# Kernel optimization log

Hardware: AMD Instinct MI355X
Metric: run time of the kernel (lower is better)

The kernel has to match this reference:

```python
import jax, jax.numpy as jnp
import numpy as np

D = 128
N = 100000
E = 500000
DIM_OUT = 2


def setup_inputs() -> dict:
    key = jax.random.key(0)
    ks = jax.random.split(key, 12)
    s = lambda d: 1.0 / np.sqrt(d)
    return {
        "x": jax.random.normal(ks[0], (N, D), jnp.float32),
        "edge_attr": jax.random.normal(ks[1], (E, D), jnp.float32),
        # node head MLP: D -> D -> DIM_OUT
        "W1": jax.random.uniform(ks[2], (D, D), jnp.float32, -s(D), s(D)),
        "b1": jnp.zeros((D,), jnp.float32),
        "W2": jax.random.uniform(ks[3], (D, DIM_OUT), jnp.float32, -s(D), s(D)),
        "b2": jnp.zeros((DIM_OUT,), jnp.float32),
        # edge aux head MLP: 3D -> 3D -> 1
        "V1": jax.random.uniform(ks[4], (3 * D, 3 * D), jnp.float32, -s(3 * D), s(3 * D)),
        "bv1": jnp.zeros((3 * D,), jnp.float32),
        "V2": jax.random.uniform(ks[5], (3 * D, 1), jnp.float32, -s(3 * D), s(3 * D)),
        "bv2": jnp.zeros((1,), jnp.float32),
        "edge_combine_weight": jnp.asarray(0.5, jnp.float32),
        "edge_index": jax.random.randint(ks[6], (2, E), 0, N, jnp.int64),
        "y": jax.random.randint(ks[7], (N,), 0, 2, jnp.int64),
        "batch_size": 50000,
    }


def reference(x, edge_attr, W1, b1, W2, b2, V1, bv1, V2, bv2,
              edge_combine_weight, edge_index, y, batch_size):
    # node classification head: 2-layer MLP
    node_logits = jax.nn.relu(x @ W1 + b1) @ W2 + b2  # [N, 2]

    src, dst = edge_index[0], edge_index[1]
    # gather src/dst node embeddings, concat edge attrs -> [E, 3D]
    edge_input = jnp.concatenate([x[src], x[dst], edge_attr], axis=-1)
    edge_scores = (jax.nn.relu(edge_input @ V1 + bv1) @ V2 + bv2)[:, 0]  # [E]
    edge_sig = jax.nn.sigmoid(edge_scores)

    # scatter-max into node slots; empty slots -> 0 (torch_scatter semantics)
    signal = jax.ops.segment_max(edge_sig, src, num_segments=N)
    signal = jnp.where(jnp.isfinite(signal), signal, 0.0)

    node_logits = node_logits.at[:, 1].add(edge_combine_weight * signal)

    pred = node_logits[:batch_size]
    label = y[:batch_size]
    return pred, label
```

## Files before the change

kernel.cpp:

```cpp
#include <hip/hip_runtime.h>
#include <hip/hip_bf16.h>

typedef __bf16 bf16;
typedef bf16 bf16x8 __attribute__((ext_vector_type(8)));
typedef float f32x4 __attribute__((ext_vector_type(4)));

#define D 128

__global__ void prep_kernel(const float* __restrict__ V1, const float* __restrict__ W1,
                            bf16* __restrict__ V1t, bf16* __restrict__ W1t) {
  int i = blockIdx.x * 256 + threadIdx.x;
  if (i < 384 * 384) { int k = i / 384, n = i % 384; V1t[n * 384 + k] = (bf16)V1[i]; }
  if (i < 128 * 128) { int k = i >> 7, n = i & 127;  W1t[n * 128 + k] = (bf16)W1[i]; }
}

__global__ void compact_kernel(const int* __restrict__ ei, int E, int bs,
                               int* __restrict__ count, int* __restrict__ list) {
  int e = blockIdx.x * 256 + threadIdx.x;
  if (e < E && ei[e] < bs) {
    int p = atomicAdd(count, 1);
    list[p] = e;
  }
}

__global__ __launch_bounds__(256, 2) void node_kernel(
    const float* __restrict__ x, const bf16* __restrict__ W1t,
    const float* __restrict__ b1, const float* __restrict__ W2,
    const float* __restrict__ b2, float* __restrict__ logits, int bs)
{
  __shared__ bf16 sA[64][136];
  __shared__ float sOut0[64], sOut1[64];

  int tid = threadIdx.x;
  if (tid < 64) { sOut0[tid] = 0.f; sOut1[tid] = 0.f; }

  {
    int g = tid >> 5, fl = tid & 31;
#pragma unroll
    for (int i = 0; i < 8; ++i) {
      int row = i * 8 + g;
      const float4* base = (const float4*)(x + (size_t)(blockIdx.x * 64 + row) * D);
      float4 v = base[fl];
      union { bf16 h[4]; uint2 u; } cv;
      cv.h[0] = (bf16)v.x; cv.h[1] = (bf16)v.y; cv.h[2] = (bf16)v.z; cv.h[3] = (bf16)v.w;
      *(uint2*)&sA[row][fl * 4] = cv.u;
    }
  }
  __syncthreads();

  int wave = tid >> 6, lane = tid & 63;
  int l15 = lane & 15, quad = lane >> 4;

  f32x4 acc[2][4];
#pragma unroll
  for (int ct = 0; ct < 2; ++ct)
#pragma unroll
    for (int rt = 0; rt < 4; ++rt)
      acc[ct][rt] = (f32x4){0.f, 0.f, 0.f, 0.f};

  for (int kc = 0; kc < 4; ++kc) {
    int k = kc * 32 + quad * 8;
    bf16x8 a[4], b[2];
#pragma unroll
    for (int rt = 0; rt < 4; ++rt)
      a[rt] = *(const bf16x8*)&sA[rt * 16 + l15][k];
#pragma unroll
    for (int ct = 0; ct < 2; ++ct)
      b[ct] = *(const bf16x8*)&W1t[(size_t)(wave * 32 + ct * 16 + l15) * 128 + k];
#pragma unroll
    for (int ct = 0; ct < 2; ++ct)
#pragma unroll
      for (int rt = 0; rt < 4; ++rt)
        acc[ct][rt] = __builtin_amdgcn_mfma_f32_16x16x32_bf16(a[rt], b[ct], acc[ct][rt], 0, 0, 0);
  }

  float bc[2], w0[2], w1[2];
#pragma unroll
  for (int ct = 0; ct < 2; ++ct) {
    int n = wave * 32 + ct * 16 + l15;
    bc[ct] = b1[n]; w0[ct] = W2[n * 2]; w1[ct] = W2[n * 2 + 1];
  }
#pragma unroll
  for (int rt = 0; rt < 4; ++rt) {
#pragma unroll
    for (int reg = 0; reg < 4; ++reg) {
      float p0 = 0.f, p1 = 0.f;
#pragma unroll
      for (int ct = 0; ct < 2; ++ct) {
        float h = fmaxf(acc[ct][rt][reg] + bc[ct], 0.f);
        p0 += h * w0[ct]; p1 += h * w1[ct];
      }
      p0 += __shfl_xor(p0, 1, 16); p0 += __shfl_xor(p0, 2, 16);
      p0 += __shfl_xor(p0, 4, 16); p0 += __shfl_xor(p0, 8, 16);
      p1 += __shfl_xor(p1, 1, 16); p1 += __shfl_xor(p1, 2, 16);
      p1 += __shfl_xor(p1, 4, 16); p1 += __shfl_xor(p1, 8, 16);
      if (l15 == 0) {
        int row = rt * 16 + quad * 4 + reg;
        atomicAdd(&sOut0[row], p0);
        atomicAdd(&sOut1[row], p1);
      }
    }
  }
  __syncthreads();
  if (tid < 64) {
    int node = blockIdx.x * 64 + tid;
    if (node < bs) {
      logits[2 * node]     = sOut0[tid] + b2[0];
      logits[2 * node + 1] = sOut1[tid] + b2[1];
    }
  }
}

__global__ __launch_bounds__(256, 2) void edge_kernel(
    const float* __restrict__ x, const float* __restrict__ ea,
    const bf16* __restrict__ V1t, const float* __restrict__ bv1,
    const float* __restrict__ V2, const float* __restrict__ bv2,
    const int* __restrict__ ei, const int* __restrict__ count,
    const int* __restrict__ list, float* __restrict__ signal,
    int E, int bs)
{
  __shared__ bf16 sA[64][392];
  __shared__ float sScore[64];
  __shared__ int sSrc[64], sDst[64], sE[64];

  int nvalid = *count - (int)(blockIdx.x * 64);
  if (nvalid <= 0) return;
  if (nvalid > 64) nvalid = 64;

  int tid = threadIdx.x;
  if (tid < 64) {
    int e = 0;
    if (tid < nvalid) e = list[blockIdx.x * 64 + tid];
    sE[tid] = e;
    sSrc[tid] = ei[e];
    sDst[tid] = ei[E + e];
    sScore[tid] = 0.f;
  }
  __syncthreads();

  {
    int g = tid >> 5, fl = tid & 31;
#pragma unroll
    for (int i = 0; i < 24; ++i) {
      int t = i * 8 + g;
      int row = t & 63, seg = t >> 6;
      const float* base;
      if (seg == 0)      base = x  + (size_t)sSrc[row] * D;
      else if (seg == 1) base = x  + (size_t)sDst[row] * D;
      else               base = ea + (size_t)sE[row]   * D;
      float4 v = ((const float4*)base)[fl];
      union { bf16 h[4]; uint2 u; } cv;
      cv.h[0] = (bf16)v.x; cv.h[1] = (bf16)v.y; cv.h[2] = (bf16)v.z; cv.h[3] = (bf16)v.w;
      *(uint2*)&sA[row][seg * 128 + fl * 4] = cv.u;
    }
  }
  __syncthreads();

  int wave = tid >> 6, lane = tid & 63;
  int l15 = lane & 15, quad = lane >> 4;

  f32x4 acc[6][4];
#pragma unroll
  for (int ct = 0; ct < 6; ++ct)
#pragma unroll
    for (int rt = 0; rt < 4; ++rt)
      acc[ct][rt] = (f32x4){0.f, 0.f, 0.f, 0.f};

  const bf16* Bbase = V1t + (size_t)(wave * 96 + l15) * 384 + quad * 8;

  for (int kc = 0; kc < 12; ++kc) {
    int k = kc * 32 + quad * 8;
    bf16x8 a[4], b[6];
#pragma unroll
    for (int rt = 0; rt < 4; ++rt)
      a[rt] = *(const bf16x8*)&sA[rt * 16 + l15][k];
#pragma unroll
    for (int ct = 0; ct < 6; ++ct)
      b[ct] = *(const bf16x8*)(Bbase + (size_t)ct * 16 * 384 + kc * 32);
#pragma unroll
    for (int ct = 0; ct < 6; ++ct)
#pragma unroll
      for (int rt = 0; rt < 4; ++rt)
        acc[ct][rt] = __builtin_amdgcn_mfma_f32_16x16x32_bf16(a[rt], b[ct], acc[ct][rt], 0, 0, 0);
  }

  float bvc[6], v2c[6];
#pragma unroll
  for (int ct = 0; ct < 6; ++ct) {
    int n = wave * 96 + ct * 16 + l15;
    bvc[ct] = bv1[n]; v2c[ct] = V2[n];
  }
#pragma unroll
  for (int rt = 0; rt < 4; ++rt) {
#pragma unroll
    for (int reg = 0; reg < 4; ++reg) {
      float p = 0.f;
#pragma unroll
      for (int ct = 0; ct < 6; ++ct)
        p += fmaxf(acc[ct][rt][reg] + bvc[ct], 0.f) * v2c[ct];
      p += __shfl_xor(p, 1, 16);
      p += __shfl_xor(p, 2, 16);
      p += __shfl_xor(p, 4, 16);
      p += __shfl_xor(p, 8, 16);
      if (l15 == 0)
        atomicAdd(&sScore[rt * 16 + quad * 4 + reg], p);
    }
  }
  __syncthreads();
  if (tid < nvalid) {
    float sc = sScore[tid] + bv2[0];
    float sig = 1.f / (1.f + __expf(-sc));
    atomicMax((int*)&signal[sSrc[tid]], __float_as_int(sig));
  }
}

__global__ void combine_kernel(const float* __restrict__ logits, const float* __restrict__ signal,
                               const int* __restrict__ y, const float* __restrict__ ecw,
                               float* __restrict__ out, int bs) {
  int i = blockIdx.x * 256 + threadIdx.x;
  if (i < bs) {
    out[2 * i]     = logits[2 * i];
    out[2 * i + 1] = logits[2 * i + 1] + ecw[0] * signal[i];
    out[2 * bs + i] = (float)y[i];
  }
}

extern "C" void kernel_launch(void* const* d_in, const int* in_sizes, int n_in,
                              void* d_out, int out_size, void* d_ws, size_t ws_size,
                              hipStream_t stream) {
  const float* x   = (const float*)d_in[0];
  const float* ea  = (const float*)d_in[1];
  const float* W1  = (const float*)d_in[2];
  const float* b1  = (const float*)d_in[3];
  const float* W2  = (const float*)d_in[4];
  const float* b2  = (const float*)d_in[5];
  const float* V1  = (const float*)d_in[6];
  const float* bv1 = (const float*)d_in[7];
  const float* V2  = (const float*)d_in[8];
  const float* bv2 = (const float*)d_in[9];
  const float* ecw = (const float*)d_in[10];
  const int*   ei  = (const int*)d_in[11];
  const int*   y   = (const int*)d_in[12];

  int E  = in_sizes[1] / D;
  int bs = out_size / 3;

  char* ws = (char*)d_ws;
  size_t off = 0;
  bf16* V1t = (bf16*)(ws + off); off += (size_t)384 * 384 * 2;
  bf16* W1t = (bf16*)(ws + off); off += (size_t)128 * 128 * 2;
  float* signal = (float*)(ws + off); off += (size_t)bs * 4;
  float* logits = (float*)(ws + off); off += (size_t)bs * 8;
  int* count = (int*)(ws + off); off += 16;
  int* list  = (int*)(ws + off); off += (size_t)E * 4;

  hipMemsetAsync(signal, 0, (size_t)bs * 4, stream);
  hipMemsetAsync(count, 0, 4, stream);

  prep_kernel<<<(384 * 384 + 255) / 256, 256, 0, stream>>>(V1, W1, V1t, W1t);
  compact_kernel<<<(E + 255) / 256, 256, 0, stream>>>(ei, E, bs, count, list);
  node_kernel<<<(bs + 63) / 64, 256, 0, stream>>>(x, W1t, b1, W2, b2, logits, bs);
  edge_kernel<<<(E + 63) / 64, 256, 0, stream>>>(x, ea, V1t, bv1, V2, bv2,
                                                 ei, count, list, signal, E, bs);
  combine_kernel<<<(bs + 255) / 256, 256, 0, stream>>>(logits, signal, y, ecw,
                                                       (float*)d_out, bs);
}
```

Before: 682.7 us.

## Fuse setup kernels and make edge kernel persistent with prefetched gathers

Merges weight prep, edge compaction, node MLP and signal zeroing into one block-partitioned setup kernel, so the node MLP transposes W1 into shared memory itself. The edge kernel becomes a persistent grid of fixed size that loops over edge tiles, double-buffering gathered indices and prefetching the next tile's edge attributes and indices while computing the current one. It also software-pipelines the V1 B-operand loads across the k loop. This targets launch overhead and exposed gather latency, at the cost of more register pressure and a fixed grid size that may underfill or overfill the GPU.

Result: slower. 697.6 us (+2.2%).

```diff
diff --git a/kernel.cpp b/kernel.cpp
--- a/kernel.cpp
+++ b/kernel.cpp
@@ -6,108 +6,119 @@
 typedef float f32x4 __attribute__((ext_vector_type(4)));
 
 #define D 128
-
-__global__ void prep_kernel(const float* __restrict__ V1, const float* __restrict__ W1,
-                            bf16* __restrict__ V1t, bf16* __restrict__ W1t) {
-  int i = blockIdx.x * 256 + threadIdx.x;
-  if (i < 384 * 384) { int k = i / 384, n = i % 384; V1t[n * 384 + k] = (bf16)V1[i]; }
-  if (i < 128 * 128) { int k = i >> 7, n = i & 127;  W1t[n * 128 + k] = (bf16)W1[i]; }
-}
-
-__global__ void compact_kernel(const int* __restrict__ ei, int E, int bs,
-                               int* __restrict__ count, int* __restrict__ list) {
-  int e = blockIdx.x * 256 + threadIdx.x;
-  if (e < E && ei[e] < bs) {
-    int p = atomicAdd(count, 1);
-    list[p] = e;
-  }
-}
-
-__global__ __launch_bounds__(256, 2) void node_kernel(
-    const float* __restrict__ x, const bf16* __restrict__ W1t,
+#define EGRID 512
+
+__global__ __launch_bounds__(256) void setup_kernel(
+    const float* __restrict__ x, const float* __restrict__ W1,
     const float* __restrict__ b1, const float* __restrict__ W2,
-    const float* __restrict__ b2, float* __restrict__ logits, int bs)
+    const float* __restrict__ b2, const float* __restrict__ V1,
+    const int* __restrict__ ei, int E, int bs,
+    bf16* __restrict__ V1t, int* __restrict__ count, int* __restrict__ list,
+    float* __restrict__ signal, float* __restrict__ logits,
+    int NN, int NT, int NC)
 {
-  __shared__ bf16 sA[64][136];
-  __shared__ float sOut0[64], sOut1[64];
-
-  int tid = threadIdx.x;
-  if (tid < 64) { sOut0[tid] = 0.f; sOut1[tid] = 0.f; }
-
-  {
-    int g = tid >> 5, fl = tid & 31;
-#pragma unroll
-    for (int i = 0; i < 8; ++i) {
-      int row = i * 8 + g;
-      const float4* base = (const float4*)(x + (size_t)(blockIdx.x * 64 + row) * D);
-      float4 v = base[fl];
-      union { bf16 h[4]; uint2 u; } cv;
-      cv.h[0] = (bf16)v.x; cv.h[1] = (bf16)v.y; cv.h[2] = (bf16)v.z; cv.h[3] = (bf16)v.w;
-      *(uint2*)&sA[row][fl * 4] = cv.u;
-    }
-  }
-  __syncthreads();
-
-  int wave = tid >> 6, lane = tid & 63;
-  int l15 = lane & 15, quad = lane >> 4;
-
-  f32x4 acc[2][4];
-#pragma unroll
-  for (int ct = 0; ct < 2; ++ct)
-#pragma unroll
-    for (int rt = 0; rt < 4; ++rt)
-      acc[ct][rt] = (f32x4){0.f, 0.f, 0.f, 0.f};
-
-  for (int kc = 0; kc < 4; ++kc) {
-    int k = kc * 32 + quad * 8;
-    bf16x8 a[4], b[2];
-#pragma unroll
-    for (int rt = 0; rt < 4; ++rt)
-      a[rt] = *(const bf16x8*)&sA[rt * 16 + l15][k];
+  __shared__ struct { bf16 A[64][136]; bf16 W[128][136]; float o0[64]; float o1[64]; } sm;
+  int bid = blockIdx.x, tid = threadIdx.x;
+
+  if (bid < NN) {
+#pragma unroll
+    for (int p = 0; p < 4; ++p) {
+      int tile = tid + p * 256;
+      int tk = tile >> 5, tn = tile & 31;
+      float4 r0 = *(const float4*)&W1[(4 * tk + 0) * D + 4 * tn];
+      float4 r1 = *(const float4*)&W1[(4 * tk + 1) * D + 4 * tn];
+      float4 r2 = *(const float4*)&W1[(4 * tk + 2) * D + 4 * tn];
+      float4 r3 = *(const float4*)&W1[(4 * tk + 3) * D + 4 * tn];
+      const float* q0 = (const float*)&r0; const float* q1 = (const float*)&r1;
+      const float* q2 = (const float*)&r2; const float* q3 = (const float*)&r3;
+#pragma unroll
+      for (int j = 0; j < 4; ++j) {
+        union { bf16 h[4]; ushort4 u; } cv;
+        cv.h[0] = (bf16)q0[j]; cv.h[1] = (bf16)q1[j];
+        cv.h[2] = (bf16)q2[j]; cv.h[3] = (bf16)q3[j];
+        *(ushort4*)&sm.W[4 * tn + j][4 * tk] = cv.u;
+      }
+    }
+    {
+      int g = tid >> 5, fl = tid & 31;
+#pragma unroll
+      for (int i = 0; i < 8; ++i) {
+        int row = i * 8 + g;
+        const float4* base = (const float4*)(x + (size_t)(bid * 64 + row) * D);
+        float4 v = base[fl];
+        union { bf16 h[4]; uint2 u; } cv;
+        cv.h[0] = (bf16)v.x; cv.h[1] = (bf16)v.y; cv.h[2] = (bf16)v.z; cv.h[3] = (bf16)v.w;
+        *(uint2*)&sm.A[row][fl * 4] = cv.u;
+      }
+    }
+    if (tid < 64) { sm.o0[tid] = 0.f; sm.o1[tid] = 0.f; }
+    __syncthreads();
+
+    int wave = tid >> 6, lane = tid & 63;
+    int l15 = lane & 15, quad = lane >> 4;
+    f32x4 acc[2][4];
 #pragma unroll
     for (int ct = 0; ct < 2; ++ct)
-      b[ct] = *(const bf16x8*)&W1t[(size_t)(wave * 32 + ct * 16 + l15) * 128 + k];
-#pragma unroll
-    for (int ct = 0; ct < 2; ++ct)
-#pragma unroll
-      for (int rt = 0; rt < 4; ++rt)
-        acc[ct][rt] = __builtin_amdgcn_mfma_f32_16x16x32_bf16(a[rt], b[ct], acc[ct][rt], 0, 0, 0);
-  }
-
-  float bc[2], w0[2], w1[2];
-#pragma unroll
-  for (int ct = 0; ct < 2; ++ct) {
-    int n = wave * 32 + ct * 16 + l15;
-    bc[ct] = b1[n]; w0[ct] = W2[n * 2]; w1[ct] = W2[n * 2 + 1];
-  }
-#pragma unroll
-  for (int rt = 0; rt < 4; ++rt) {
-#pragma unroll
-    for (int reg = 0; reg < 4; ++reg) {
-      float p0 = 0.f, p1 = 0.f;
-#pragma unroll
-      for (int ct = 0; ct < 2; ++ct) {
-        float h = fmaxf(acc[ct][rt][reg] + bc[ct], 0.f);
-        p0 += h * w0[ct]; p1 += h * w1[ct];
-      }
-      p0 += __shfl_xor(p0, 1, 16); p0 += __shfl_xor(p0, 2, 16);
-      p0 += __shfl_xor(p0, 4, 16); p0 += __shfl_xor(p0, 8, 16);
-      p1 += __shfl_xor(p1, 1, 16); p1 += __shfl_xor(p1, 2, 16);
-      p1 += __shfl_xor(p1, 4, 16); p1 += __shfl_xor(p1, 8, 16);
-      if (l15 == 0) {
-        int row = rt * 16 + quad * 4 + reg;
-        atomicAdd(&sOut0[row], p0);
-        atomicAdd(&sOut1[row], p1);
-      }
-    }
-  }
-  __syncthreads();
-  if (tid < 64) {
-    int node = blockIdx.x * 64 + tid;
-    if (node < bs) {
-      logits[2 * node]     = sOut0[tid] + b2[0];
-      logits[2 * node + 1] = sOut1[tid] + b2[1];
-    }
+#pragma unroll
+      for (int rt = 0; rt < 4; ++rt) acc[ct][rt] = (f32x4){0.f, 0.f, 0.f, 0.f};
+    for (int kc = 0; kc < 4; ++kc) {
+      int k = kc * 32 + quad * 8;
+      bf16x8 a[4], b[2];
+#pragma unroll
+      for (int rt = 0; rt < 4; ++rt) a[rt] = *(const bf16x8*)&sm.A[rt * 16 + l15][k];
+#pragma unroll
+      for (int ct = 0; ct < 2; ++ct) b[ct] = *(const bf16x8*)&sm.W[wave * 32 + ct * 16 + l15][k];
+#pragma unroll
+      for (int ct = 0; ct < 2; ++ct)
+#pragma unroll
+        for (int rt = 0; rt < 4; ++rt)
+          acc[ct][rt] = __builtin_amdgcn_mfma_f32_16x16x32_bf16(a[rt], b[ct], acc[ct][rt], 0, 0, 0);
+    }
+    float bc[2], w0[2], w1[2];
+#pragma unroll
+    for (int ct = 0; ct < 2; ++ct) {
+      int n = wave * 32 + ct * 16 + l15;
+      bc[ct] = b1[n]; w0[ct] = W2[n * 2]; w1[ct] = W2[n * 2 + 1];
+    }
+#pragma unroll
+    for (int rt = 0; rt < 4; ++rt) {
+#pragma unroll
+      for (int reg = 0; reg < 4; ++reg) {
+        float p0 = 0.f, p1 = 0.f;
+#pragma unroll
+        for (int ct = 0; ct < 2; ++ct) {
+          float h = fmaxf(acc[ct][rt][reg] + bc[ct], 0.f);
+          p0 += h * w0[ct]; p1 += h * w1[ct];
+        }
+        p0 += __shfl_xor(p0, 1, 16); p0 += __shfl_xor(p0, 2, 16);
+        p0 += __shfl_xor(p0, 4, 16); p0 += __shfl_xor(p0, 8, 16);
+        p1 += __shfl_xor(p1, 1, 16); p1 += __shfl_xor(p1, 2, 16);
+        p1 += __shfl_xor(p1, 4, 16); p1 += __shfl_xor(p1, 8, 16);
+        if (l15 == 0) {
+          int row = rt * 16 + quad * 4 + reg;
+          atomicAdd(&sm.o0[row], p0);
+          atomicAdd(&sm.o1[row], p1);
+        }
+      }
+    }
+    __syncthreads();
+    if (tid < 64) {
+      int node = bid * 64 + tid;
+      if (node < bs) {
+        logits[2 * node]     = sm.o0[tid] + b2[0];
+        logits[2 * node + 1] = sm.o1[tid] + b2[1];
+      }
+    }
+  } else if (bid < NN + NT) {
+    int i = (bid - NN) * 256 + tid;
+    int k = i / 384, n = i - k * 384;
+    V1t[n * 384 + k] = (bf16)V1[i];
+  } else if (bid < NN + NT + NC) {
+    int e = (bid - NN - NT) * 256 + tid;
+    if (e < E && ei[e] < bs) { int p = atomicAdd(count, 1); list[p] = e; }
+  } else {
+    int i = (bid - NN - NT - NC) * 256 + tid;
+    if (i < bs) signal[i] = 0.f;
   }
 }
 
@@ -120,97 +131,165 @@
     int E, int bs)
 {
   __shared__ bf16 sA[64][392];
+  __shared__ int sIdx[2][3][64];
   __shared__ float sScore[64];
-  __shared__ int sSrc[64], sDst[64], sE[64];
-
-  int nvalid = *count - (int)(blockIdx.x * 64);
-  if (nvalid <= 0) return;
-  if (nvalid > 64) nvalid = 64;
-
-  int tid = threadIdx.x;
-  if (tid < 64) {
-    int e = 0;
-    if (tid < nvalid) e = list[blockIdx.x * 64 + tid];
-    sE[tid] = e;
-    sSrc[tid] = ei[e];
-    sDst[tid] = ei[E + e];
-    sScore[tid] = 0.f;
+
+  const int live = *count;
+  const int nT = (live + 63) >> 6;
+  const int bid0 = blockIdx.x;
+  if (bid0 >= nT) return;
+  const int stride = gridDim.x;
+  const int tid = threadIdx.x;
+  const int g = tid >> 5, fl = tid & 31;
+
+  if (tid < 64) sScore[tid] = 0.f;
+  if (tid < 128) {
+    int slot = tid >> 6, r = tid & 63;
+    int tt = bid0 + slot * stride;
+    int e = 0, s = 0, d = 0;
+    if (tt < nT) {
+      int gi = tt * 64 + r;
+      if (gi < live) { e = list[gi]; s = ei[e]; d = ei[E + e]; }
+    }
+    sIdx[slot][0][r] = s; sIdx[slot][1][r] = d; sIdx[slot][2][r] = e;
+  }
+  int eReg = 0;
+  {
+    int t2 = bid0 + 2 * stride;
+    if (tid < 64 && t2 < nT) {
+      int gi = t2 * 64 + tid;
+      if (gi < live) eReg = list[gi];
+    }
   }
   __syncthreads();
 
-  {
-    int g = tid >> 5, fl = tid & 31;
-#pragma unroll
-    for (int i = 0; i < 24; ++i) {
-      int t = i * 8 + g;
-      int row = t & 63, seg = t >> 6;
-      const float* base;
-      if (seg == 0)      base = x  + (size_t)sSrc[row] * D;
-      else if (seg == 1) base = x  + (size_t)sDst[row] * D;
-      else               base = ea + (size_t)sE[row]   * D;
-      float4 v = ((const float4*)base)[fl];
-      union { bf16 h[4]; uint2 u; } cv;
-      cv.h[0] = (bf16)v.x; cv.h[1] = (bf16)v.y; cv.h[2] = (bf16)v.z; cv.h[3] = (bf16)v.w;
-      *(uint2*)&sA[row][seg * 128 + fl * 4] = cv.u;
-    }
-  }
-  __syncthreads();
-
-  int wave = tid >> 6, lane = tid & 63;
-  int l15 = lane & 15, quad = lane >> 4;
-
-  f32x4 acc[6][4];
-#pragma unroll
-  for (int ct = 0; ct < 6; ++ct)
-#pragma unroll
-    for (int rt = 0; rt < 4; ++rt)
-      acc[ct][rt] = (f32x4){0.f, 0.f, 0.f, 0.f};
-
+  float4 Rea[8];
+#pragma unroll
+  for (int i = 0; i < 8; ++i) {
+    int r = i * 8 + g;
+    int e = sIdx[0][2][r];
+    Rea[i] = ((const float4*)(ea + (size_t)e * D))[fl];
+  }
+
+  const int wave = tid >> 6, lane = tid & 63;
+  const int l15 = lane & 15, quad = lane >> 4;
   const bf16* Bbase = V1t + (size_t)(wave * 96 + l15) * 384 + quad * 8;
-
-  for (int kc = 0; kc < 12; ++kc) {
-    int k = kc * 32 + quad * 8;
-    bf16x8 a[4], b[6];
-#pragma unroll
-    for (int rt = 0; rt < 4; ++rt)
-      a[rt] = *(const bf16x8*)&sA[rt * 16 + l15][k];
-#pragma unroll
-    for (int ct = 0; ct < 6; ++ct)
-      b[ct] = *(const bf16x8*)(Bbase + (size_t)ct * 16 * 384 + kc * 32);
-#pragma unroll
-    for (int ct = 0; ct < 6; ++ct)
-#pragma unroll
-      for (int rt = 0; rt < 4; ++rt)
-        acc[ct][rt] = __builtin_amdgcn_mfma_f32_16x16x32_bf16(a[rt], b[ct], acc[ct][rt], 0, 0, 0);
-  }
-
   float bvc[6], v2c[6];
 #pragma unroll
   for (int ct = 0; ct < 6; ++ct) {
     int n = wave * 96 + ct * 16 + l15;
     bvc[ct] = bv1[n]; v2c[ct] = V2[n];
   }
-#pragma unroll
-  for (int rt = 0; rt < 4; ++rt) {
-#pragma unroll
-    for (int reg = 0; reg < 4; ++reg) {
-      float p = 0.f;
+
+  int it = 0;
+  for (int t = bid0; t < nT; t += stride, ++it) {
+    const int P = it & 1;
+    const bool hasN = (t + stride) < nT;
+    const bool has2 = (t + 2 * stride) < nT;
+    const bool has3 = (t + 3 * stride) < nT;
+
+    __syncthreads();
+
+#pragma unroll
+    for (int i = 0; i < 8; ++i) {
+      int r = i * 8 + g;
+      union { bf16 h[4]; uint2 u; } cv;
+      cv.h[0] = (bf16)Rea[i].x; cv.h[1] = (bf16)Rea[i].y;
+      cv.h[2] = (bf16)Rea[i].z; cv.h[3] = (bf16)Rea[i].w;
+      *(uint2*)&sA[r][256 + fl * 4] = cv.u;
+    }
+    float4 Rx[16];
+#pragma unroll
+    for (int i = 0; i < 16; ++i) {
+      int tt2 = i * 8 + g;
+      int r = tt2 & 63, seg = tt2 >> 6;
+      int idx = sIdx[P][seg][r];
+      Rx[i] = ((const float4*)(x + (size_t)idx * D))[fl];
+    }
+    if (hasN) {
+#pragma unroll
+      for (int i = 0; i < 8; ++i) {
+        int r = i * 8 + g;
+        int e = sIdx[P ^ 1][2][r];
+        Rea[i] = ((const float4*)(ea + (size_t)e * D))[fl];
+      }
+    }
+    int sN = 0, dN = 0, eSv = eReg;
+    if (tid < 64) {
+      if (has2) { sN = ei[eSv]; dN = ei[E + eSv]; }
+      eReg = 0;
+      if (has3) {
+        int gi = (t + 3 * stride) * 64 + tid;
+        if (gi < live) eReg = list[gi];
+      }
+    }
+    int srcCur = sIdx[P][0][tid & 63];
+#pragma unroll
+    for (int i = 0; i < 16; ++i) {
+      int tt2 = i * 8 + g;
+      int r = tt2 & 63, seg = tt2 >> 6;
+      union { bf16 h[4]; uint2 u; } cv;
+      cv.h[0] = (bf16)Rx[i].x; cv.h[1] = (bf16)Rx[i].y;
+      cv.h[2] = (bf16)Rx[i].z; cv.h[3] = (bf16)Rx[i].w;
+      *(uint2*)&sA[r][seg * 128 + fl * 4] = cv.u;
+    }
+    __syncthreads();
+
+    f32x4 acc[6][4];
+#pragma unroll
+    for (int ct = 0; ct < 6; ++ct)
+#pragma unroll
+      for (int rt = 0; rt < 4; ++rt) acc[ct][rt] = (f32x4){0.f, 0.f, 0.f, 0.f};
+
+    bf16x8 bCur[6], bNxt[6];
+#pragma unroll
+    for (int ct = 0; ct < 6; ++ct)
+      bCur[ct] = *(const bf16x8*)(Bbase + (size_t)ct * 16 * 384);
+    for (int kc = 0; kc < 12; ++kc) {
+      bf16x8 a[4];
+      int k = kc * 32 + quad * 8;
+#pragma unroll
+      for (int rt = 0; rt < 4; ++rt)
+        a[rt] = *(const bf16x8*)&sA[rt * 16 + l15][k];
+      if (kc < 11) {
+#pragma unroll
+        for (int ct = 0; ct < 6; ++ct)
+          bNxt[ct] = *(const bf16x8*)(Bbase + (size_t)ct * 16 * 384 + (kc + 1) * 32);
+      }
 #pragma unroll
       for (int ct = 0; ct < 6; ++ct)
-        p += fmaxf(acc[ct][rt][reg] + bvc[ct], 0.f) * v2c[ct];
-      p += __shfl_xor(p, 1, 16);
-      p += __shfl_xor(p, 2, 16);
-      p += __shfl_xor(p, 4, 16);
-      p += __shfl_xor(p, 8, 16);
-      if (l15 == 0)
-        atomicAdd(&sScore[rt * 16 + quad * 4 + reg], p);
-    }
-  }
-  __syncthreads();
-  if (tid < nvalid) {
-    float sc = sScore[tid] + bv2[0];
-    float sig = 1.f / (1.f + __expf(-sc));
-    atomicMax((int*)&signal[sSrc[tid]], __float_as_int(sig));
+#pragma unroll
+        for (int rt = 0; rt < 4; ++rt)
+          acc[ct][rt] = __builtin_amdgcn_mfma_f32_16x16x32_bf16(a[rt], bCur[ct], acc[ct][rt], 0, 0, 0);
+#pragma unroll
+      for (int ct = 0; ct < 6; ++ct) bCur[ct] = bNxt[ct];
+    }
+
+#pragma unroll
+    for (int rt = 0; rt < 4; ++rt) {
+#pragma unroll
+      for (int reg = 0; reg < 4; ++reg) {
+        float p = 0.f;
+#pragma unroll
+        for (int ct = 0; ct < 6; ++ct)
+          p += fmaxf(acc[ct][rt][reg] + bvc[ct], 0.f) * v2c[ct];
+        p += __shfl_xor(p, 1, 16); p += __shfl_xor(p, 2, 16);
+        p += __shfl_xor(p, 4, 16); p += __shfl_xor(p, 8, 16);
+        if (l15 == 0) atomicAdd(&sScore[rt * 16 + quad * 4 + reg], p);
+      }
+    }
+    if (tid < 64 && has2) {
+      sIdx[P][0][tid] = sN; sIdx[P][1][tid] = dN; sIdx[P][2][tid] = eSv;
+    }
+    __syncthreads();
+    if (tid < 64) {
+      if ((t * 64 + tid) < live) {
+        float sc = sScore[tid] + bv2[0];
+        float sig = 1.f / (1.f + __expf(-sc));
+        atomicMax((int*)&signal[srcCur], __float_as_int(sig));
+      }
+      sScore[tid] = 0.f;
+    }
   }
 }
 
@@ -219,8 +298,8 @@
                                float* __restrict__ out, int bs) {
   int i = blockIdx.x * 256 + threadIdx.x;
   if (i < bs) {
-    out[2 * i]     = logits[2 * i];
-    out[2 * i + 1] = logits[2 * i + 1] + ecw[0] * signal[i];
+    out[2 * i]      = logits[2 * i];
+    out[2 * i + 1]  = logits[2 * i + 1] + ecw[0] * signal[i];
     out[2 * bs + i] = (float)y[i];
   }
 }
@@ -248,20 +327,21 @@
   char* ws = (char*)d_ws;
   size_t off = 0;
   bf16* V1t = (bf16*)(ws + off); off += (size_t)384 * 384 * 2;
-  bf16* W1t = (bf16*)(ws + off); off += (size_t)128 * 128 * 2;
   float* signal = (float*)(ws + off); off += (size_t)bs * 4;
   float* logits = (float*)(ws + off); off += (size_t)bs * 8;
   int* count = (int*)(ws + off); off += 16;
   int* list  = (int*)(ws + off); off += (size_t)E * 4;
 
-  hipMemsetAsync(signal, 0, (size_t)bs * 4, stream);
+  int NN = (bs + 63) / 64;
+  int NT = (384 * 384) / 256;
+  int NC = (E + 255) / 256;
+  int NZ = (bs + 255) / 256;
+
   hipMemsetAsync(count, 0, 4, stream);
-
-  prep_kernel<<<(384 * 384 + 255) / 256, 256, 0, stream>>>(V1, W1, V1t, W1t);
-  compact_kernel<<<(E + 255) / 256, 256, 0, stream>>>(ei, E, bs, count, list);
-  node_kernel<<<(bs + 63) / 64, 256, 0, stream>>>(x, W1t, b1, W2, b2, logits, bs);
-  edge_kernel<<<(E + 63) / 64, 256, 0, stream>>>(x, ea, V1t, bv1, V2, bv2,
-                                                 ei, count, list, signal, E, bs);
+  setup_kernel<<<NN + NT + NC + NZ, 256, 0, stream>>>(
+      x, W1, b1, W2, b2, V1, ei, E, bs, V1t, count, list, signal, logits, NN, NT, NC);
+  edge_kernel<<<EGRID, 256, 0, stream>>>(x, ea, V1t, bv1, V2, bv2,
+                                         ei, count, list, signal, E, bs);
   combine_kernel<<<(bs + 255) / 256, 256, 0, stream>>>(logits, signal, y, ecw,
                                                        (float*)d_out, bs);
 }
```
